# Performance work log

Measured on AMD Instinct MI355X. Metric: run time of the kernel, lower is better.

The kernel has to match this reference:

```python
import jax, jax.numpy as jnp
import numpy as np

TEMPERATURE = 0.07


def setup_inputs() -> dict:
    key = jax.random.key(0)
    k1, k2 = jax.random.split(key)
    B, D = 8192, 128
    z_i = jax.random.normal(k1, (B, D), dtype=jnp.float32)
    z_j = jax.random.normal(k2, (B, D), dtype=jnp.float32)
    return {"z_i": z_i, "z_j": z_j}


def reference(z_i, z_j):
    B = z_i.shape[0]
    # L2-normalize each embedding (F.normalize with eps=1e-12 clamp)
    def l2norm(x):
        n = jnp.linalg.norm(x, axis=1, keepdims=True)
        return x / jnp.maximum(n, 1e-12)
    reps = jnp.concatenate([l2norm(z_i), l2norm(z_j)], axis=0)  # [2B, D]
    sim = jnp.matmul(reps, reps.T) / TEMPERATURE  # [2B, 2B]
    # NOTE: original code applies CrossEntropyLoss to exp(sim/T) values,
    # i.e. the logits themselves are the exponentiated similarities.
    e = jnp.exp(sim)
    N = 2 * B
    idx = jnp.arange(N)
    # CE with the positive placed first and all non-diagonal entries as logits:
    # loss_i = logsumexp(nondiag row) - positive_logit
    neg_inf = jnp.asarray(-jnp.inf, dtype=e.dtype)
    row_logits = jnp.where(idx[None, :] == idx[:, None], neg_inf, e)  # mask diagonal
    lse = jax.scipy.special.logsumexp(row_logits, axis=1)  # [2B]
    pos_idx = jnp.where(idx < B, idx + B, idx - B)
    pos = e[idx, pos_idx]  # [2B]
    return jnp.mean(lse - pos)
```

## Files before the change

### kernel.cpp

```cpp
#include <hip/hip_runtime.h>
#include <hip/hip_bf16.h>


#define NROWS 16384
#define BHALF 8192
#define DDIM  128
#define TILE  128
#define ROWS_PER_BLOCK 256
#define NSPLIT 8
#define COLS_PER_SPLIT (NROWS / NSPLIT)
#define NITERS (COLS_PER_SPLIT / TILE)
#define LDS_STRIDE 136
#define LOG2E 1.4426950408889634f
#define C_EXP (LOG2E / 0.07f)
#define NEGBIG -1.0e30f

typedef __attribute__((ext_vector_type(8))) short bf16x8;
typedef __attribute__((ext_vector_type(4))) float f32x4;

__device__ inline unsigned short f2bf(float x) {
    unsigned int b = __float_as_uint(x);
    b += 0x7FFFu + ((b >> 16) & 1u);
    return (unsigned short)(b >> 16);
}
__device__ inline float bflo(unsigned int u) { return __uint_as_float(u << 16); }
__device__ inline float bfhi(unsigned int u) { return __uint_as_float(u & 0xFFFF0000u); }

__global__ void norm_kernel(const float* __restrict__ zi, const float* __restrict__ zj,
                            unsigned short* __restrict__ repsB,
                            unsigned short* __restrict__ repsA,
                            float* __restrict__ out) {
    int w = threadIdx.x >> 6;
    int lane = threadIdx.x & 63;
    int row = blockIdx.x * 4 + w;
    const float* src = (row < BHALF) ? (zi + (size_t)row * DDIM)
                                     : (zj + (size_t)(row - BHALF) * DDIM);
    float2 v = ((const float2*)src)[lane];
    float ss = v.x * v.x + v.y * v.y;
    #pragma unroll
    for (int d = 1; d < 64; d <<= 1) ss += __shfl_xor(ss, d, 64);
    float inv = 1.0f / fmaxf(sqrtf(ss), 1e-12f);
    float x = v.x * inv, y = v.y * inv;
    unsigned int pb = (unsigned int)f2bf(x) | ((unsigned int)f2bf(y) << 16);
    unsigned int pa = (unsigned int)f2bf(x * C_EXP) | ((unsigned int)f2bf(y * C_EXP) << 16);
    ((unsigned int*)repsB)[(size_t)row * (DDIM / 2) + lane] = pb;
    ((unsigned int*)repsA)[(size_t)row * (DDIM / 2) + lane] = pa;
    if (blockIdx.x == 0 && threadIdx.x == 0) out[0] = 0.0f;
}

template <bool DIAG>
__device__ __forceinline__ void tile_compute(const unsigned short* lds,
                                             const bf16x8 (&afrag)[4][4],
                                             float (&A1)[4][4], float (&A2)[4][4],
                                             int rowBase, int colBase,
                                             int laneLo, int quad) {
    #pragma unroll
    for (int c8 = 0; c8 < 8; ++c8) {
        bf16x8 bfrag[4];
        int brow = c8 * 16 + laneLo;
        #pragma unroll
        for (int kt = 0; kt < 4; ++kt)
            bfrag[kt] = *(const bf16x8*)(&lds[brow * LDS_STRIDE + kt * 32 + quad * 8]);
        #pragma unroll
        for (int rt = 0; rt < 4; ++rt) {
            f32x4 acc = (f32x4){0.f, 0.f, 0.f, 0.f};
            #pragma unroll
            for (int kt = 0; kt < 4; ++kt)
                acc = __builtin_amdgcn_mfma_f32_16x16x32_bf16(
                    afrag[rt][kt], bfrag[kt], acc, 0, 0, 0);
            #pragma unroll
            for (int rg = 0; rg < 4; ++rg) {
                float a = acc[rg];
                if (DIAG) {
                    int drel = rowBase + rt * 16 + quad * 4 + rg - colBase - laneLo;
                    a = (drel == c8 * 16) ? NEGBIG : a;
                }
                float mn = fminf(a, A1[rt][rg]);
                A2[rt][rg] = fmaxf(A2[rt][rg], mn);
                A1[rt][rg] = fmaxf(A1[rt][rg], a);
            }
        }
    }
}

__global__ __launch_bounds__(256, 2)
void ntx_main(const unsigned short* __restrict__ repsA,
              const unsigned short* __restrict__ repsB,
              float2* __restrict__ part) {
    __shared__ unsigned short lds[TILE * LDS_STRIDE];
    const int tid = threadIdx.x;
    const int w = tid >> 6, lane = tid & 63;
    const int laneLo = lane & 15, quad = lane >> 4;
    const int bx = blockIdx.x, by = blockIdx.y;
    const int rowBase = bx * ROWS_PER_BLOCK + w * 64;

    bf16x8 afrag[4][4];
    #pragma unroll
    for (int rt = 0; rt < 4; ++rt)
        #pragma unroll
        for (int kt = 0; kt < 4; ++kt) {
            int r = rowBase + rt * 16 + laneLo;
            int k = kt * 32 + quad * 8;
            afrag[rt][kt] = *(const bf16x8*)(repsA + (size_t)r * DDIM + k);
        }

    float A1[4][4], A2[4][4];
    #pragma unroll
    for (int rt = 0; rt < 4; ++rt)
        #pragma unroll
        for (int rg = 0; rg < 4; ++rg) { A1[rt][rg] = NEGBIG; A2[rt][rg] = NEGBIG; }

    const int colBase0 = by * COLS_PER_SPLIT;
    const uint4* repsV = (const uint4*)repsB;

    for (int it = 0; it < NITERS; ++it) {
        int colBase = colBase0 + it * TILE;
        __syncthreads();
        #pragma unroll
        for (int i = 0; i < 8; ++i) {
            int idx = tid + i * 256;
            int r = idx >> 4, c = idx & 15;
            uint4 v = repsV[(size_t)(colBase + r) * 16 + c];
            *(uint4*)(&lds[r * LDS_STRIDE + c * 8]) = v;
        }
        __syncthreads();

        if ((rowBase >> 7) == (colBase >> 7))
            tile_compute<true>(lds, afrag, A1, A2, rowBase, colBase, laneLo, quad);
        else
            tile_compute<false>(lds, afrag, A1, A2, rowBase, colBase, laneLo, quad);
    }

    #pragma unroll
    for (int rt = 0; rt < 4; ++rt)
        #pragma unroll
        for (int rg = 0; rg < 4; ++rg) {
            float m1 = A1[rt][rg], m2 = A2[rt][rg];
            #pragma unroll
            for (int d = 1; d < 16; d <<= 1) {
                float m1o = __shfl_xor(m1, d, 64);
                float m2o = __shfl_xor(m2, d, 64);
                m2 = fmaxf(fmaxf(m2, m2o), fminf(m1, m1o));
                m1 = fmaxf(m1, m1o);
            }
            if (laneLo == 0) {
                int gr = rowBase + rt * 16 + quad * 4 + rg;
                part[(size_t)gr * NSPLIT + by] = make_float2(m1, m2);
            }
        }
}

__global__ void finish_kernel(const unsigned short* __restrict__ repsB,
                              const float2* __restrict__ part,
                              float* __restrict__ out) {
    int row = blockIdx.x * 256 + threadIdx.x;
    int prow = (row < BHALF) ? row + BHALF : row - BHALF;
    const uint4* rv = (const uint4*)repsB + (size_t)row * 16;
    const uint4* pv = (const uint4*)repsB + (size_t)prow * 16;
    float dot = 0.0f;
    #pragma unroll
    for (int c = 0; c < 16; ++c) {
        uint4 a = rv[c], b = pv[c];
        dot = fmaf(bflo(a.x), bflo(b.x), dot); dot = fmaf(bfhi(a.x), bfhi(b.x), dot);
        dot = fmaf(bflo(a.y), bflo(b.y), dot); dot = fmaf(bfhi(a.y), bfhi(b.y), dot);
        dot = fmaf(bflo(a.z), bflo(b.z), dot); dot = fmaf(bfhi(a.z), bfhi(b.z), dot);
        dot = fmaf(bflo(a.w), bflo(b.w), dot); dot = fmaf(bfhi(a.w), bfhi(b.w), dot);
    }
    float pos = __builtin_amdgcn_exp2f(dot * C_EXP);

    float M1 = NEGBIG, M2 = NEGBIG;
    #pragma unroll
    for (int k = 0; k < NSPLIT; ++k) {
        float2 p = part[(size_t)row * NSPLIT + k];
        M2 = fmaxf(fmaxf(M2, p.y), fminf(M1, p.x));
        M1 = fmaxf(M1, p.x);
    }
    float e1 = __builtin_amdgcn_exp2f(M1);
    float e2 = __builtin_amdgcn_exp2f(M2);
    float lse = e1 + log1pf(__builtin_amdgcn_exp2f((e2 - e1) * LOG2E));
    float v = lse - pos;

    #pragma unroll
    for (int d = 1; d < 64; d <<= 1) v += __shfl_xor(v, d, 64);
    __shared__ float red[4];
    int lane = threadIdx.x & 63, w = threadIdx.x >> 6;
    if (lane == 0) red[w] = v;
    __syncthreads();
    if (threadIdx.x == 0)
        atomicAdd(out, (red[0] + red[1] + red[2] + red[3]) * (1.0f / NROWS));
}

extern "C" void kernel_launch(void* const* d_in, const int* in_sizes, int n_in,
                              void* d_out, int out_size, void* d_ws, size_t ws_size,
                              hipStream_t stream) {
    const float* zi = (const float*)d_in[0];
    const float* zj = (const float*)d_in[1];
    float* out = (float*)d_out;
    unsigned short* repsB = (unsigned short*)d_ws;
    unsigned short* repsA = repsB + (size_t)NROWS * DDIM;
    float2* part = (float2*)((char*)d_ws + 2 * (size_t)NROWS * DDIM * 2);

    norm_kernel<<<NROWS / 4, 256, 0, stream>>>(zi, zj, repsB, repsA, out);
    ntx_main<<<dim3(NROWS / ROWS_PER_BLOCK, NSPLIT), 256, 0, stream>>>(repsA, repsB, part);
    finish_kernel<<<NROWS / 256, 256, 0, stream>>>(repsB, part, out);
}
```

Measured before the change: 137.5 us.

## Exploit similarity matrix symmetry by computing only upper-triangular block pairs

```diff
diff --git a/kernel.cpp b/kernel.cpp
--- a/kernel.cpp
+++ b/kernel.cpp
@@ -6,10 +6,8 @@
 #define BHALF 8192
 #define DDIM  128
 #define TILE  128
-#define ROWS_PER_BLOCK 256
-#define NSPLIT 8
-#define COLS_PER_SPLIT (NROWS / NSPLIT)
-#define NITERS (COLS_PER_SPLIT / TILE)
+#define NSB   64
+#define NSLOT 64
 #define LDS_STRIDE 136
 #define LOG2E 1.4426950408889634f
 #define C_EXP (LOG2E / 0.07f)
@@ -23,12 +21,9 @@
     b += 0x7FFFu + ((b >> 16) & 1u);
     return (unsigned short)(b >> 16);
 }
-__device__ inline float bflo(unsigned int u) { return __uint_as_float(u << 16); }
-__device__ inline float bfhi(unsigned int u) { return __uint_as_float(u & 0xFFFF0000u); }
 
 __global__ void norm_kernel(const float* __restrict__ zi, const float* __restrict__ zj,
-                            unsigned short* __restrict__ repsB,
-                            unsigned short* __restrict__ repsA,
+                            unsigned short* __restrict__ reps,
                             float* __restrict__ out) {
     int w = threadIdx.x >> 6;
     int lane = threadIdx.x & 63;
@@ -39,28 +34,30 @@
     float ss = v.x * v.x + v.y * v.y;
     #pragma unroll
     for (int d = 1; d < 64; d <<= 1) ss += __shfl_xor(ss, d, 64);
-    float inv = 1.0f / fmaxf(sqrtf(ss), 1e-12f);
-    float x = v.x * inv, y = v.y * inv;
-    unsigned int pb = (unsigned int)f2bf(x) | ((unsigned int)f2bf(y) << 16);
-    unsigned int pa = (unsigned int)f2bf(x * C_EXP) | ((unsigned int)f2bf(y * C_EXP) << 16);
-    ((unsigned int*)repsB)[(size_t)row * (DDIM / 2) + lane] = pb;
-    ((unsigned int*)repsA)[(size_t)row * (DDIM / 2) + lane] = pa;
+    const float S = sqrtf(C_EXP);
+    float inv = S / fmaxf(sqrtf(ss), 1e-12f);
+    unsigned int pb = (unsigned int)f2bf(v.x * inv) | ((unsigned int)f2bf(v.y * inv) << 16);
+    ((unsigned int*)reps)[(size_t)row * (DDIM / 2) + lane] = pb;
     if (blockIdx.x == 0 && threadIdx.x == 0) out[0] = 0.0f;
 }
 
-template <bool DIAG>
-__device__ __forceinline__ void tile_compute(const unsigned short* lds,
-                                             const bf16x8 (&afrag)[4][4],
-                                             float (&A1)[4][4], float (&A2)[4][4],
-                                             int rowBase, int colBase,
-                                             int laneLo, int quad) {
+template <int MODE>
+__device__ __forceinline__ void tile_compute(
+    const unsigned short* __restrict__ lds,
+    const bf16x8 (&afrag)[4][4],
+    float (&A1)[4][4], float (&A2)[4][4],
+    float2* __restrict__ colSlot,
+    float* __restrict__ pos,
+    int rowBaseG, int colBaseG,
+    int rowRel, int laneLo, int quad) {
     #pragma unroll
     for (int c8 = 0; c8 < 8; ++c8) {
         bf16x8 bfrag[4];
-        int brow = c8 * 16 + laneLo;
+        const int brow = c8 * 16 + laneLo;
         #pragma unroll
         for (int kt = 0; kt < 4; ++kt)
             bfrag[kt] = *(const bf16x8*)(&lds[brow * LDS_STRIDE + kt * 32 + quad * 8]);
+        float c1 = NEGBIG, c2 = NEGBIG;
         #pragma unroll
         for (int rt = 0; rt < 4; ++rt) {
             f32x4 acc = (f32x4){0.f, 0.f, 0.f, 0.f};
@@ -71,37 +68,60 @@
             #pragma unroll
             for (int rg = 0; rg < 4; ++rg) {
                 float a = acc[rg];
-                if (DIAG) {
-                    int drel = rowBase + rt * 16 + quad * 4 + rg - colBase - laneLo;
-                    a = (drel == c8 * 16) ? NEGBIG : a;
+                if (MODE) {
+                    int rel = rowRel + rt * 16 + quad * 4 + rg - laneLo;
+                    bool hit = (rel == c8 * 16);
+                    if (MODE == 1) {
+                        a = hit ? NEGBIG : a;
+                    } else if (hit) {
+                        pos[rowBaseG + rt * 16 + quad * 4 + rg] = a;
+                        pos[colBaseG + c8 * 16 + laneLo] = a;
+                    }
                 }
                 float mn = fminf(a, A1[rt][rg]);
+                A1[rt][rg] = fmaxf(A1[rt][rg], a);
                 A2[rt][rg] = fmaxf(A2[rt][rg], mn);
-                A1[rt][rg] = fmaxf(A1[rt][rg], a);
+                float mc = fminf(a, c1);
+                c1 = fmaxf(c1, a);
+                c2 = fmaxf(c2, mc);
             }
         }
+        #pragma unroll
+        for (int d = 16; d < 64; d <<= 1) {
+            float c1o = __shfl_xor(c1, d, 64);
+            float c2o = __shfl_xor(c2, d, 64);
+            c2 = fmaxf(fmaxf(c2, c2o), fminf(c1, c1o));
+            c1 = fmaxf(c1, c1o);
+        }
+        if (quad == 0) colSlot[c8 * 16 + laneLo] = make_float2(c1, c2);
     }
 }
 
 __global__ __launch_bounds__(256, 2)
-void ntx_main(const unsigned short* __restrict__ repsA,
-              const unsigned short* __restrict__ repsB,
-              float2* __restrict__ part) {
+void ntx_main(const unsigned short* __restrict__ reps,
+              float2* __restrict__ part, float* __restrict__ pos) {
     __shared__ unsigned short lds[TILE * LDS_STRIDE];
+    __shared__ float2 colBuf[4][256];
     const int tid = threadIdx.x;
     const int w = tid >> 6, lane = tid & 63;
     const int laneLo = lane & 15, quad = lane >> 4;
-    const int bx = blockIdx.x, by = blockIdx.y;
-    const int rowBase = bx * ROWS_PER_BLOCK + w * 64;
+
+    int t = (int)blockIdx.x, bi = 0;
+    while (t >= NSB - bi) { t -= NSB - bi; ++bi; }
+    const int bj = bi + t;
+    const int rowBlk = bi * 256, colBlk = bj * 256;
+    const int rowBaseG = rowBlk + w * 64;
+    const int rowRel = (w & 1) * 64;
+    const int mySub = w >> 1;
 
     bf16x8 afrag[4][4];
     #pragma unroll
     for (int rt = 0; rt < 4; ++rt)
         #pragma unroll
         for (int kt = 0; kt < 4; ++kt) {
-            int r = rowBase + rt * 16 + laneLo;
+            int r = rowBaseG + rt * 16 + laneLo;
             int k = kt * 32 + quad * 8;
-            afrag[rt][kt] = *(const bf16x8*)(repsA + (size_t)r * DDIM + k);
+            afrag[rt][kt] = *(const bf16x8*)(reps + (size_t)r * DDIM + k);
         }
 
     float A1[4][4], A2[4][4];
@@ -110,25 +130,32 @@
         #pragma unroll
         for (int rg = 0; rg < 4; ++rg) { A1[rt][rg] = NEGBIG; A2[rt][rg] = NEGBIG; }
 
-    const int colBase0 = by * COLS_PER_SPLIT;
-    const uint4* repsV = (const uint4*)repsB;
-
-    for (int it = 0; it < NITERS; ++it) {
-        int colBase = colBase0 + it * TILE;
+    const uint4* repsV = (const uint4*)reps;
+
+    #pragma unroll
+    for (int ct = 0; ct < 2; ++ct) {
+        int colBaseG = colBlk + ct * TILE;
         __syncthreads();
         #pragma unroll
         for (int i = 0; i < 8; ++i) {
             int idx = tid + i * 256;
             int r = idx >> 4, c = idx & 15;
-            uint4 v = repsV[(size_t)(colBase + r) * 16 + c];
+            uint4 v = repsV[(size_t)(colBaseG + r) * 16 + c];
             *(uint4*)(&lds[r * LDS_STRIDE + c * 8]) = v;
         }
         __syncthreads();
 
-        if ((rowBase >> 7) == (colBase >> 7))
-            tile_compute<true>(lds, afrag, A1, A2, rowBase, colBase, laneLo, quad);
+        float2* colSlot = &colBuf[w][ct * TILE];
+        bool spec = (mySub == ct);
+        if (bi == bj && spec)
+            tile_compute<1>(lds, afrag, A1, A2, colSlot, pos, rowBaseG, colBaseG,
+                            rowRel, laneLo, quad);
+        else if (bj == bi + 32 && spec)
+            tile_compute<2>(lds, afrag, A1, A2, colSlot, pos, rowBaseG, colBaseG,
+                            rowRel, laneLo, quad);
         else
-            tile_compute<false>(lds, afrag, A1, A2, rowBase, colBase, laneLo, quad);
+            tile_compute<0>(lds, afrag, A1, A2, colSlot, pos, rowBaseG, colBaseG,
+                            rowRel, laneLo, quad);
     }
 
     #pragma unroll
@@ -144,41 +171,40 @@
                 m1 = fmaxf(m1, m1o);
             }
             if (laneLo == 0) {
-                int gr = rowBase + rt * 16 + quad * 4 + rg;
-                part[(size_t)gr * NSPLIT + by] = make_float2(m1, m2);
+                int gr = rowBaseG + rt * 16 + quad * 4 + rg;
+                part[(size_t)gr * NSLOT + bj] = make_float2(m1, m2);
             }
         }
-}
-
-__global__ void finish_kernel(const unsigned short* __restrict__ repsB,
-                              const float2* __restrict__ part,
+
+    __syncthreads();
+    if (bi != bj) {
+        float2 p0 = colBuf[0][tid], p1 = colBuf[1][tid];
+        float2 p2 = colBuf[2][tid], p3 = colBuf[3][tid];
+        float C1 = p0.x, C2 = p0.y;
+        C2 = fmaxf(fmaxf(C2, p1.y), fminf(C1, p1.x)); C1 = fmaxf(C1, p1.x);
+        C2 = fmaxf(fmaxf(C2, p2.y), fminf(C1, p2.x)); C1 = fmaxf(C1, p2.x);
+        C2 = fmaxf(fmaxf(C2, p3.y), fminf(C1, p3.x)); C1 = fmaxf(C1, p3.x);
+        part[(size_t)(colBlk + tid) * NSLOT + bi] = make_float2(C1, C2);
+    }
+}
+
+__global__ void finish_kernel(const float2* __restrict__ part,
+                              const float* __restrict__ pos,
                               float* __restrict__ out) {
     int row = blockIdx.x * 256 + threadIdx.x;
-    int prow = (row < BHALF) ? row + BHALF : row - BHALF;
-    const uint4* rv = (const uint4*)repsB + (size_t)row * 16;
-    const uint4* pv = (const uint4*)repsB + (size_t)prow * 16;
-    float dot = 0.0f;
-    #pragma unroll
-    for (int c = 0; c < 16; ++c) {
-        uint4 a = rv[c], b = pv[c];
-        dot = fmaf(bflo(a.x), bflo(b.x), dot); dot = fmaf(bfhi(a.x), bfhi(b.x), dot);
-        dot = fmaf(bflo(a.y), bflo(b.y), dot); dot = fmaf(bfhi(a.y), bfhi(b.y), dot);
-        dot = fmaf(bflo(a.z), bflo(b.z), dot); dot = fmaf(bfhi(a.z), bfhi(b.z), dot);
-        dot = fmaf(bflo(a.w), bflo(b.w), dot); dot = fmaf(bfhi(a.w), bfhi(b.w), dot);
-    }
-    float pos = __builtin_amdgcn_exp2f(dot * C_EXP);
-
+    const float4* p4 = (const float4*)(part + (size_t)row * NSLOT);
     float M1 = NEGBIG, M2 = NEGBIG;
     #pragma unroll
-    for (int k = 0; k < NSPLIT; ++k) {
-        float2 p = part[(size_t)row * NSPLIT + k];
-        M2 = fmaxf(fmaxf(M2, p.y), fminf(M1, p.x));
-        M1 = fmaxf(M1, p.x);
+    for (int k = 0; k < NSLOT / 2; ++k) {
+        float4 p = p4[k];
+        M2 = fmaxf(fmaxf(M2, p.y), fminf(M1, p.x)); M1 = fmaxf(M1, p.x);
+        M2 = fmaxf(fmaxf(M2, p.w), fminf(M1, p.z)); M1 = fmaxf(M1, p.z);
     }
     float e1 = __builtin_amdgcn_exp2f(M1);
     float e2 = __builtin_amdgcn_exp2f(M2);
+    float posv = __builtin_amdgcn_exp2f(pos[row]);
     float lse = e1 + log1pf(__builtin_amdgcn_exp2f((e2 - e1) * LOG2E));
-    float v = lse - pos;
+    float v = lse - posv;
 
     #pragma unroll
     for (int d = 1; d < 64; d <<= 1) v += __shfl_xor(v, d, 64);
@@ -196,11 +222,12 @@
     const float* zi = (const float*)d_in[0];
     const float* zj = (const float*)d_in[1];
     float* out = (float*)d_out;
-    unsigned short* repsB = (unsigned short*)d_ws;
-    unsigned short* repsA = repsB + (size_t)NROWS * DDIM;
-    float2* part = (float2*)((char*)d_ws + 2 * (size_t)NROWS * DDIM * 2);
-
-    norm_kernel<<<NROWS / 4, 256, 0, stream>>>(zi, zj, repsB, repsA, out);
-    ntx_main<<<dim3(NROWS / ROWS_PER_BLOCK, NSPLIT), 256, 0, stream>>>(repsA, repsB, part);
-    finish_kernel<<<NROWS / 256, 256, 0, stream>>>(repsB, part, out);
-}
+    unsigned short* reps = (unsigned short*)d_ws;
+    float2* part = (float2*)((char*)d_ws + (size_t)NROWS * DDIM * 2);
+    float* pos = (float*)((char*)d_ws + (size_t)NROWS * DDIM * 2
+                          + (size_t)NROWS * NSLOT * sizeof(float2));
+
+    norm_kernel<<<NROWS / 4, 256, 0, stream>>>(zi, zj, reps, out);
+    ntx_main<<<NSB * (NSB + 1) / 2, 256, 0, stream>>>(reps, part, pos);
+    finish_kernel<<<NROWS / 256, 256, 0, stream>>>(part, pos, out);
+}
```

After: 156.0 us. 13.4% more time.
